# Optimization experiments

Hardware: AMD Instinct MI355X
Metric: run time of the kernel (lower is better)

The kernel has to match this reference:

```python
import jax, jax.numpy as jnp
import numpy as np

BATCH, SEQLEN, D_MODEL, D_STATE = 2, 2048, 512, 64
DT_MIN, DT_MAX = 1e-4, 1e-3


def setup_inputs() -> dict:
    key = jax.random.key(0)
    k1, k2, k3, k4 = jax.random.split(key, 4)
    u = jax.random.normal(k1, (BATCH, SEQLEN, D_MODEL), dtype=jnp.float32)
    # real parts of the complex params B, C (imag parts never affect the output)
    B_re = (jax.random.normal(k2, (D_STATE,), dtype=jnp.float32) / np.float32(np.sqrt(D_STATE)))
    C_re = (jax.random.normal(k3, (D_STATE,), dtype=jnp.float32) / np.float32(np.sqrt(D_STATE)))
    log_dt = jax.random.uniform(k4, (D_MODEL,), minval=np.log(DT_MIN), maxval=np.log(DT_MAX)).astype(jnp.float32)
    D = jnp.ones((D_MODEL,), dtype=jnp.float32)
    return {"u": u, "B_re": B_re, "C_re": C_re, "log_dt": log_dt, "D": D}


def reference(u, B_re, C_re, log_dt, D):
    # u: [B, L, H]; B_re/C_re: [N]; log_dt/D: [H]
    N = B_re.shape[0]
    # buffer: log_A = -0.5 * log(1 + n/N), n = 1..N  (A = exp(log_A) in (0,1])
    log_A = -0.5 * jnp.log1p(jnp.arange(1, N + 1, dtype=jnp.float32) / N)
    A = jnp.exp(log_A)                       # [N]
    delta = jnp.exp(log_dt)                  # [H]
    A_d = jnp.exp(delta[:, None] * A[None, :])          # [H, N]
    B_d = (A_d - 1.0) * B_re[None, :] * delta[:, None]  # [H, N]

    Bsz, L, H = u.shape
    x0 = jnp.zeros((Bsz, H, N), dtype=u.dtype)

    def step(x, u_t):                        # x: [B,H,N], u_t: [B,H]
        x = A_d * x + B_d * u_t[..., None]
        y_t = jnp.einsum('bhn,n->bh', x, C_re) + D * u_t
        return x, y_t

    _, ys = jax.lax.scan(step, x0, jnp.swapaxes(u, 0, 1))  # ys: [L,B,H]
    return jnp.swapaxes(ys, 0, 1)                          # [B,L,H]
```

## Files before the change

kernel.cpp:

```cpp
#include <hip/hip_runtime.h>
#include <math.h>


#define BATCH   2
#define SEQLEN  2048
#define DMODEL  512
#define DSTATE  64
#define T_CHUNK 64
#define NCHUNK  (SEQLEN / T_CHUNK)
#define RT      8

__device__ __forceinline__ float A_cont(int n) {
    return rsqrtf(1.0f + (float)(n + 1) * (1.0f / 64.0f));
}

__global__ __launch_bounds__(256) void k_setup(const float* __restrict__ B_re,
                                               const float* __restrict__ C_re,
                                               const float* __restrict__ log_dt,
                                               const float* __restrict__ D,
                                               float* __restrict__ Kbuf,
                                               float* __restrict__ AdTab,
                                               float* __restrict__ CpowStep) {
    int g = blockIdx.x * blockDim.x + threadIdx.x;
    int h = g & (DMODEL - 1);
    int j = g >> 9;
    float delta = expf(log_dt[h]);
    float dAj = delta * A_cont(j);
    float Adj = expf(dAj);
    AdTab[j * DMODEL + h] = Adj;
    float e8 = Adj * Adj; e8 = e8 * e8; e8 = e8 * e8;
    float p = C_re[j] * Adj;
    #pragma unroll
    for (int i = 0; i < RT; ++i) {
        CpowStep[(i * DSTATE + j) * DMODEL + h] = p;
        p *= e8;
    }
    float acc = (j == 0) ? D[h] : 0.0f;
    for (int n = 0; n < DSTATE; ++n) {
        float dAn = delta * A_cont(n);
        float Bd = expm1f(dAn) * B_re[n] * delta;
        acc = fmaf(C_re[n] * Bd, expf(dAn * (float)j), acc);
    }
    Kbuf[(8 + j) * DMODEL + h] = acc;
    if (j < 8) Kbuf[j * DMODEL + h] = 0.0f;
}

__global__ __launch_bounds__(256) void k_xlocal(const float* __restrict__ u,
                                                const float* __restrict__ B_re,
                                                const float* __restrict__ log_dt,
                                                float* __restrict__ xl) {
    int g = blockIdx.x * blockDim.x + threadIdx.x;
    int lane = g & 63;
    int w = g >> 6;
    int hb = w & 7;
    int ng = (w >> 3) & 7;
    int c  = (w >> 6) & (NCHUNK - 1);
    int b  = w >> 11;
    int h = hb * 64 + lane;
    float delta = expf(log_dt[h]);
    float Ad[8], Bd[8], x[8];
    #pragma unroll
    for (int nn = 0; nn < 8; ++nn) {
        int n = ng * 8 + nn;
        float dA = delta * A_cont(n);
        Ad[nn] = expf(dA);
        Bd[nn] = expm1f(dA) * B_re[n] * delta;
        x[nn] = 0.0f;
    }
    const float* up = u + ((size_t)(b * SEQLEN + c * T_CHUNK)) * DMODEL + h;
    #pragma unroll 4
    for (int s = 0; s < T_CHUNK; ++s) {
        float uv = up[(size_t)s * DMODEL];
        #pragma unroll
        for (int nn = 0; nn < 8; ++nn)
            x[nn] = fmaf(Ad[nn], x[nn], Bd[nn] * uv);
    }
    float* xp = xl + ((size_t)((b * NCHUNK + c) * DSTATE + ng * 8)) * DMODEL + h;
    #pragma unroll
    for (int nn = 0; nn < 8; ++nn) xp[(size_t)nn * DMODEL] = x[nn];
}

__global__ __launch_bounds__(256) void k_scan(const float* __restrict__ log_dt,
                                              float* __restrict__ xl) {
    int g = blockIdx.x * blockDim.x + threadIdx.x;
    int h = g & (DMODEL - 1);
    int n = (g >> 9) & (DSTATE - 1);
    int b = g >> 15;
    float delta = expf(log_dt[h]);
    float ApT = expf(delta * A_cont(n) * (float)T_CHUNK);
    float s = 0.0f;
    float* base = xl + ((size_t)(b * NCHUNK * DSTATE + n)) * DMODEL + h;
    for (int cm1 = 0; cm1 < NCHUNK - 1; ++cm1) {
        float v = base[(size_t)cm1 * DSTATE * DMODEL];
        s = fmaf(ApT, s, v);
        base[(size_t)cm1 * DSTATE * DMODEL] = s;
    }
}

__global__ __launch_bounds__(256) void k_out(const float* __restrict__ u,
                                             const float* __restrict__ Kbuf,
                                             const float* __restrict__ AdTab,
                                             const float* __restrict__ CpowStep,
                                             const float* __restrict__ Sbuf,
                                             float* __restrict__ out) {
    int g = blockIdx.x * blockDim.x + threadIdx.x;
    int h  = g & (DMODEL - 1);
    int it = (g >> 9) & 7;
    int c  = (g >> 12) & (NCHUNK - 1);
    int b  = g >> 17;
    int tp0 = it * RT;

    const float* ubase = u + ((size_t)(b * SEQLEN + c * T_CHUNK)) * DMODEL + h;
    const float* kb = Kbuf + h;

    float acc[RT], kreg[RT];
    #pragma unroll
    for (int i = 0; i < RT; ++i) {
        acc[i] = 0.0f;
        kreg[i] = kb[(size_t)(8 + tp0 + i) * DMODEL];
    }

    for (int s8 = 0; s8 <= it; ++s8) {
        #pragma unroll
        for (int q = 0; q < 8; ++q) {
            int s = s8 * 8 + q;
            float uv = ubase[(size_t)s * DMODEL];
            #pragma unroll
            for (int i = 0; i < RT; ++i) acc[i] = fmaf(kreg[i], uv, acc[i]);
            #pragma unroll
            for (int i = RT - 1; i > 0; --i) kreg[i] = kreg[i - 1];
            kreg[0] = kb[(size_t)(8 + tp0 - s - 1) * DMODEL];
        }
    }

    if (c > 0) {
        const float* sp = Sbuf + ((size_t)((b * NCHUNK + (c - 1)) * DSTATE)) * DMODEL + h;
        const float* ap = AdTab + h;
        const float* cp = CpowStep + (size_t)(it * DSTATE) * DMODEL + h;
        #pragma unroll 4
        for (int n = 0; n < DSTATE; ++n) {
            float Sv  = sp[(size_t)n * DMODEL];
            float Adv = ap[(size_t)n * DMODEL];
            float w   = cp[(size_t)n * DMODEL] * Sv;
            acc[0] += w;
            #pragma unroll
            for (int i = 1; i < RT; ++i) { w *= Adv; acc[i] += w; }
        }
    }

    float* ob = out + ((size_t)(b * SEQLEN + c * T_CHUNK + tp0)) * DMODEL + h;
    #pragma unroll
    for (int i = 0; i < RT; ++i) ob[(size_t)i * DMODEL] = acc[i];
}

extern "C" void kernel_launch(void* const* d_in, const int* in_sizes, int n_in,
                              void* d_out, int out_size, void* d_ws, size_t ws_size,
                              hipStream_t stream) {
    const float* u      = (const float*)d_in[0];
    const float* B_re   = (const float*)d_in[1];
    const float* C_re   = (const float*)d_in[2];
    const float* log_dt = (const float*)d_in[3];
    const float* D      = (const float*)d_in[4];
    float* out = (float*)d_out;
    float* ws  = (float*)d_ws;

    float* Kbuf     = ws;
    float* AdTab    = ws + 36864;
    float* CpowStep = ws + 36864 + 32768;
    float* xl       = ws + 36864 + 32768 + 262144;

    k_setup <<<128, 256, 0, stream>>>(B_re, C_re, log_dt, D, Kbuf, AdTab, CpowStep);
    k_xlocal<<<1024, 256, 0, stream>>>(u, B_re, log_dt, xl);
    k_scan  <<<256, 256, 0, stream>>>(log_dt, xl);
    k_out   <<<1024, 256, 0, stream>>>(u, Kbuf, AdTab, CpowStep, xl, out);
}
```

Baseline: 109.7 us.

## Merge setup and local-scan kernels, batch scan loads, vectorize output with float2

Merges the coefficient-setup and per-chunk local-state kernels into one launch, using block index ranges to pick the role, which removes one launch and its inter-kernel gap. The chunk scan now loads all chunk values into registers before the serial recurrence and stores them afterward, so memory latency is no longer paid inside the dependent loop. The output kernel has each thread handle two adjacent channels with float2 loads and stores, halving the thread count and widening memory accesses, at the cost of more registers per thread and fewer waves.

```diff
diff --git a/kernel.cpp b/kernel.cpp
--- a/kernel.cpp
+++ b/kernel.cpp
@@ -9,92 +9,99 @@
 #define T_CHUNK 64
 #define NCHUNK  (SEQLEN / T_CHUNK)
 #define RT      8
+#define HP      2
 
 __device__ __forceinline__ float A_cont(int n) {
     return rsqrtf(1.0f + (float)(n + 1) * (1.0f / 64.0f));
 }
 
-__global__ __launch_bounds__(256) void k_setup(const float* __restrict__ B_re,
-                                               const float* __restrict__ C_re,
-                                               const float* __restrict__ log_dt,
-                                               const float* __restrict__ D,
-                                               float* __restrict__ Kbuf,
-                                               float* __restrict__ AdTab,
-                                               float* __restrict__ CpowStep) {
-    int g = blockIdx.x * blockDim.x + threadIdx.x;
-    int h = g & (DMODEL - 1);
-    int j = g >> 9;
-    float delta = expf(log_dt[h]);
-    float dAj = delta * A_cont(j);
-    float Adj = expf(dAj);
-    AdTab[j * DMODEL + h] = Adj;
-    float e8 = Adj * Adj; e8 = e8 * e8; e8 = e8 * e8;
-    float p = C_re[j] * Adj;
-    #pragma unroll
-    for (int i = 0; i < RT; ++i) {
-        CpowStep[(i * DSTATE + j) * DMODEL + h] = p;
-        p *= e8;
+__global__ __launch_bounds__(256) void k_prep(const float* __restrict__ u,
+                                              const float* __restrict__ B_re,
+                                              const float* __restrict__ C_re,
+                                              const float* __restrict__ log_dt,
+                                              const float* __restrict__ D,
+                                              float* __restrict__ Kbuf,
+                                              float* __restrict__ AdTab,
+                                              float* __restrict__ CpowStep,
+                                              float* __restrict__ xl) {
+    if (blockIdx.x < 128) {
+        int g = blockIdx.x * 256 + threadIdx.x;
+        int h = g & (DMODEL - 1);
+        int j = g >> 9;
+        float delta = expf(log_dt[h]);
+        float dAj = delta * A_cont(j);
+        float Adj = expf(dAj);
+        AdTab[j * DMODEL + h] = Adj;
+        float e8 = Adj * Adj; e8 = e8 * e8; e8 = e8 * e8;
+        float p = C_re[j] * Adj;
+        #pragma unroll
+        for (int i = 0; i < RT; ++i) {
+            CpowStep[(i * DSTATE + j) * DMODEL + h] = p;
+            p *= e8;
+        }
+        float acc = (j == 0) ? D[h] : 0.0f;
+        for (int n = 0; n < DSTATE; ++n) {
+            float dAn = delta * A_cont(n);
+            float Bd = expm1f(dAn) * B_re[n] * delta;
+            acc = fmaf(C_re[n] * Bd, expf(dAn * (float)j), acc);
+        }
+        Kbuf[(8 + j) * DMODEL + h] = acc;
+        if (j < 8) Kbuf[j * DMODEL + h] = 0.0f;
+    } else {
+        int g = (blockIdx.x - 128) * 256 + threadIdx.x;
+        int lane = g & 63;
+        int w = g >> 6;
+        int hb = w & 7;
+        int ng = (w >> 3) & 7;
+        int c  = (w >> 6) & (NCHUNK - 1);
+        int b  = w >> 11;
+        int h = hb * 64 + lane;
+        float delta = expf(log_dt[h]);
+        float Ad[8], Bd[8], x[8];
+        #pragma unroll
+        for (int nn = 0; nn < 8; ++nn) {
+            int n = ng * 8 + nn;
+            float dA = delta * A_cont(n);
+            Ad[nn] = expf(dA);
+            Bd[nn] = expm1f(dA) * B_re[n] * delta;
+            x[nn] = 0.0f;
+        }
+        const float* up = u + ((size_t)(b * SEQLEN + c * T_CHUNK)) * DMODEL + h;
+        #pragma unroll 4
+        for (int s = 0; s < T_CHUNK; ++s) {
+            float uv = up[(size_t)s * DMODEL];
+            #pragma unroll
+            for (int nn = 0; nn < 8; ++nn)
+                x[nn] = fmaf(Ad[nn], x[nn], Bd[nn] * uv);
+        }
+        float* xp = xl + ((size_t)((b * NCHUNK + c) * DSTATE + ng * 8)) * DMODEL + h;
+        #pragma unroll
+        for (int nn = 0; nn < 8; ++nn) xp[(size_t)nn * DMODEL] = x[nn];
     }
-    float acc = (j == 0) ? D[h] : 0.0f;
-    for (int n = 0; n < DSTATE; ++n) {
-        float dAn = delta * A_cont(n);
-        float Bd = expm1f(dAn) * B_re[n] * delta;
-        acc = fmaf(C_re[n] * Bd, expf(dAn * (float)j), acc);
-    }
-    Kbuf[(8 + j) * DMODEL + h] = acc;
-    if (j < 8) Kbuf[j * DMODEL + h] = 0.0f;
-}
-
-__global__ __launch_bounds__(256) void k_xlocal(const float* __restrict__ u,
-                                                const float* __restrict__ B_re,
-                                                const float* __restrict__ log_dt,
-                                                float* __restrict__ xl) {
-    int g = blockIdx.x * blockDim.x + threadIdx.x;
-    int lane = g & 63;
-    int w = g >> 6;
-    int hb = w & 7;
-    int ng = (w >> 3) & 7;
-    int c  = (w >> 6) & (NCHUNK - 1);
-    int b  = w >> 11;
-    int h = hb * 64 + lane;
-    float delta = expf(log_dt[h]);
-    float Ad[8], Bd[8], x[8];
-    #pragma unroll
-    for (int nn = 0; nn < 8; ++nn) {
-        int n = ng * 8 + nn;
-        float dA = delta * A_cont(n);
-        Ad[nn] = expf(dA);
-        Bd[nn] = expm1f(dA) * B_re[n] * delta;
-        x[nn] = 0.0f;
-    }
-    const float* up = u + ((size_t)(b * SEQLEN + c * T_CHUNK)) * DMODEL + h;
-    #pragma unroll 4
-    for (int s = 0; s < T_CHUNK; ++s) {
-        float uv = up[(size_t)s * DMODEL];
-        #pragma unroll
-        for (int nn = 0; nn < 8; ++nn)
-            x[nn] = fmaf(Ad[nn], x[nn], Bd[nn] * uv);
-    }
-    float* xp = xl + ((size_t)((b * NCHUNK + c) * DSTATE + ng * 8)) * DMODEL + h;
-    #pragma unroll
-    for (int nn = 0; nn < 8; ++nn) xp[(size_t)nn * DMODEL] = x[nn];
 }
 
 __global__ __launch_bounds__(256) void k_scan(const float* __restrict__ log_dt,
                                               float* __restrict__ xl) {
-    int g = blockIdx.x * blockDim.x + threadIdx.x;
+    int g = blockIdx.x * 256 + threadIdx.x;
     int h = g & (DMODEL - 1);
     int n = (g >> 9) & (DSTATE - 1);
     int b = g >> 15;
     float delta = expf(log_dt[h]);
     float ApT = expf(delta * A_cont(n) * (float)T_CHUNK);
+    float* base = xl + ((size_t)(b * NCHUNK * DSTATE + n)) * DMODEL + h;
+    float v[NCHUNK - 1];
+    #pragma unroll
+    for (int c = 0; c < NCHUNK - 1; ++c)
+        v[c] = base[(size_t)c * DSTATE * DMODEL];
     float s = 0.0f;
-    float* base = xl + ((size_t)(b * NCHUNK * DSTATE + n)) * DMODEL + h;
-    for (int cm1 = 0; cm1 < NCHUNK - 1; ++cm1) {
-        float v = base[(size_t)cm1 * DSTATE * DMODEL];
-        s = fmaf(ApT, s, v);
-        base[(size_t)cm1 * DSTATE * DMODEL] = s;
+    #pragma unroll
+    for (int c = 0; c < NCHUNK - 1; ++c) {
+        s = fmaf(ApT, s, v[c]);
+        v[c] = s;
     }
+    #pragma unroll
+    for (int c = 0; c < NCHUNK - 1; ++c)
+        base[(size_t)c * DSTATE * DMODEL] = v[c];
 }
 
 __global__ __launch_bounds__(256) void k_out(const float* __restrict__ u,
@@ -103,54 +110,63 @@
                                              const float* __restrict__ CpowStep,
                                              const float* __restrict__ Sbuf,
                                              float* __restrict__ out) {
-    int g = blockIdx.x * blockDim.x + threadIdx.x;
-    int h  = g & (DMODEL - 1);
-    int it = (g >> 9) & 7;
-    int c  = (g >> 12) & (NCHUNK - 1);
-    int b  = g >> 17;
+    int g = blockIdx.x * 256 + threadIdx.x;
+    int h2 = g & 255;
+    int it = (g >> 8) & 7;
+    int c  = (g >> 11) & (NCHUNK - 1);
+    int b  = g >> 16;
+    int h = h2 * 2;
     int tp0 = it * RT;
+    const int S2 = DMODEL / 2;
 
-    const float* ubase = u + ((size_t)(b * SEQLEN + c * T_CHUNK)) * DMODEL + h;
-    const float* kb = Kbuf + h;
+    const float2* ub = (const float2*)(u + ((size_t)(b * SEQLEN + c * T_CHUNK)) * DMODEL + h);
+    const float2* kb = (const float2*)(Kbuf + h);
 
-    float acc[RT], kreg[RT];
+    float2 acc[RT], kreg[RT];
     #pragma unroll
     for (int i = 0; i < RT; ++i) {
-        acc[i] = 0.0f;
-        kreg[i] = kb[(size_t)(8 + tp0 + i) * DMODEL];
+        acc[i] = make_float2(0.0f, 0.0f);
+        kreg[i] = kb[(size_t)(8 + tp0 + i) * S2];
     }
 
     for (int s8 = 0; s8 <= it; ++s8) {
         #pragma unroll
         for (int q = 0; q < 8; ++q) {
             int s = s8 * 8 + q;
-            float uv = ubase[(size_t)s * DMODEL];
+            float2 uv = ub[(size_t)s * S2];
             #pragma unroll
-            for (int i = 0; i < RT; ++i) acc[i] = fmaf(kreg[i], uv, acc[i]);
+            for (int i = 0; i < RT; ++i) {
+                acc[i].x = fmaf(kreg[i].x, uv.x, acc[i].x);
+                acc[i].y = fmaf(kreg[i].y, uv.y, acc[i].y);
+            }
             #pragma unroll
             for (int i = RT - 1; i > 0; --i) kreg[i] = kreg[i - 1];
-            kreg[0] = kb[(size_t)(8 + tp0 - s - 1) * DMODEL];
+            kreg[0] = kb[(size_t)(8 + tp0 - s - 1) * S2];
         }
     }
 
     if (c > 0) {
-        const float* sp = Sbuf + ((size_t)((b * NCHUNK + (c - 1)) * DSTATE)) * DMODEL + h;
-        const float* ap = AdTab + h;
-        const float* cp = CpowStep + (size_t)(it * DSTATE) * DMODEL + h;
+        const float2* sp = (const float2*)(Sbuf + ((size_t)((b * NCHUNK + (c - 1)) * DSTATE)) * DMODEL + h);
+        const float2* ap = (const float2*)(AdTab + h);
+        const float2* cp = (const float2*)(CpowStep + (size_t)(it * DSTATE) * DMODEL + h);
         #pragma unroll 4
         for (int n = 0; n < DSTATE; ++n) {
-            float Sv  = sp[(size_t)n * DMODEL];
-            float Adv = ap[(size_t)n * DMODEL];
-            float w   = cp[(size_t)n * DMODEL] * Sv;
-            acc[0] += w;
+            float2 Sv  = sp[(size_t)n * S2];
+            float2 Adv = ap[(size_t)n * S2];
+            float2 Cv  = cp[(size_t)n * S2];
+            float2 w = make_float2(Cv.x * Sv.x, Cv.y * Sv.y);
+            acc[0].x += w.x; acc[0].y += w.y;
             #pragma unroll
-            for (int i = 1; i < RT; ++i) { w *= Adv; acc[i] += w; }
+            for (int i = 1; i < RT; ++i) {
+                w.x *= Adv.x; w.y *= Adv.y;
+                acc[i].x += w.x; acc[i].y += w.y;
+            }
         }
     }
 
-    float* ob = out + ((size_t)(b * SEQLEN + c * T_CHUNK + tp0)) * DMODEL + h;
+    float2* ob = (float2*)(out + ((size_t)(b * SEQLEN + c * T_CHUNK + tp0)) * DMODEL + h);
     #pragma unroll
-    for (int i = 0; i < RT; ++i) ob[(size_t)i * DMODEL] = acc[i];
+    for (int i = 0; i < RT; ++i) ob[(size_t)i * S2] = acc[i];
 }
 
 extern "C" void kernel_launch(void* const* d_in, const int* in_sizes, int n_in,
@@ -169,8 +185,7 @@
     float* CpowStep = ws + 36864 + 32768;
     float* xl       = ws + 36864 + 32768 + 262144;
 
-    k_setup <<<128, 256, 0, stream>>>(B_re, C_re, log_dt, D, Kbuf, AdTab, CpowStep);
-    k_xlocal<<<1024, 256, 0, stream>>>(u, B_re, log_dt, xl);
-    k_scan  <<<256, 256, 0, stream>>>(log_dt, xl);
-    k_out   <<<1024, 256, 0, stream>>>(u, Kbuf, AdTab, CpowStep, xl, out);
+    k_prep<<<1152, 256, 0, stream>>>(u, B_re, C_re, log_dt, D, Kbuf, AdTab, CpowStep, xl);
+    k_scan<<<256, 256, 0, stream>>>(log_dt, xl);
+    k_out <<<512, 256, 0, stream>>>(u, Kbuf, AdTab, CpowStep, xl, out);
 }
```

Result: no change. 109.1 us (-0.6%).

## Fuse SSM setup, chunk scan and output into one cooperative kernel

Applied to the files above, without the earlier changes.

Replaces the four separate launches (setup, local chunk states, inter-chunk scan, output) with a single cooperative kernel using grid-wide syncs, cutting launch overhead and inter-kernel gaps. Each thread now handles 16 states or 16 output timesteps instead of 8, halving the grid to 512 blocks. The inter-chunk scan loads all chunk values into registers before the recurrence. The causal convolution is restructured into register-blocked 16x16 tiles. The risks are higher register pressure under launch_bounds(256,2), the cost of the grid syncs, and lower parallelism.

```diff
diff --git a/kernel.cpp b/kernel.cpp
--- a/kernel.cpp
+++ b/kernel.cpp
@@ -1,5 +1,8 @@
 #include <hip/hip_runtime.h>
+#include <hip/hip_cooperative_groups.h>
 #include <math.h>
+
+namespace cg = cooperative_groups;
 
 
 #define BATCH   2
@@ -7,150 +10,156 @@
 #define DMODEL  512
 #define DSTATE  64
 #define T_CHUNK 64
-#define NCHUNK  (SEQLEN / T_CHUNK)
-#define RT      8
+#define NCHUNK  32
+#define RT      16
 
 __device__ __forceinline__ float A_cont(int n) {
     return rsqrtf(1.0f + (float)(n + 1) * (1.0f / 64.0f));
 }
 
-__global__ __launch_bounds__(256) void k_setup(const float* __restrict__ B_re,
-                                               const float* __restrict__ C_re,
-                                               const float* __restrict__ log_dt,
-                                               const float* __restrict__ D,
-                                               float* __restrict__ Kbuf,
-                                               float* __restrict__ AdTab,
-                                               float* __restrict__ CpowStep) {
-    int g = blockIdx.x * blockDim.x + threadIdx.x;
-    int h = g & (DMODEL - 1);
-    int j = g >> 9;
-    float delta = expf(log_dt[h]);
-    float dAj = delta * A_cont(j);
-    float Adj = expf(dAj);
-    AdTab[j * DMODEL + h] = Adj;
-    float e8 = Adj * Adj; e8 = e8 * e8; e8 = e8 * e8;
-    float p = C_re[j] * Adj;
-    #pragma unroll
-    for (int i = 0; i < RT; ++i) {
-        CpowStep[(i * DSTATE + j) * DMODEL + h] = p;
-        p *= e8;
+__global__ __launch_bounds__(256, 2) void k_fused(const float* __restrict__ u,
+                                                  const float* __restrict__ B_re,
+                                                  const float* __restrict__ C_re,
+                                                  const float* __restrict__ log_dt,
+                                                  const float* __restrict__ Dp,
+                                                  float* __restrict__ Kbuf,
+                                                  float* __restrict__ AdTab,
+                                                  float* __restrict__ CpStep,
+                                                  float* __restrict__ xl,
+                                                  float* __restrict__ out) {
+    cg::grid_group grid = cg::this_grid();
+    int tid = blockIdx.x * 256 + threadIdx.x;
+
+    {
+        int h  = tid & (DMODEL - 1);
+        int ng = (tid >> 9) & 3;
+        int c  = (tid >> 11) & (NCHUNK - 1);
+        int b  = tid >> 16;
+        float delta = expf(log_dt[h]);
+        float Ad[16], Bd[16], x[16];
+        #pragma unroll
+        for (int nn = 0; nn < 16; ++nn) {
+            int n = ng * 16 + nn;
+            float dA = delta * A_cont(n);
+            Ad[nn] = expf(dA);
+            Bd[nn] = expm1f(dA) * B_re[n] * delta;
+            x[nn] = 0.0f;
+        }
+        const float* up = u + ((size_t)(b * SEQLEN + c * T_CHUNK)) * DMODEL + h;
+        #pragma unroll 4
+        for (int s = 0; s < T_CHUNK; ++s) {
+            float uv = up[(size_t)s * DMODEL];
+            #pragma unroll
+            for (int nn = 0; nn < 16; ++nn)
+                x[nn] = fmaf(Ad[nn], x[nn], Bd[nn] * uv);
+        }
+        float* xp = xl + ((size_t)((b * NCHUNK + c) * DSTATE + ng * 16)) * DMODEL + h;
+        #pragma unroll
+        for (int nn = 0; nn < 16; ++nn) xp[(size_t)nn * DMODEL] = x[nn];
     }
-    float acc = (j == 0) ? D[h] : 0.0f;
-    for (int n = 0; n < DSTATE; ++n) {
-        float dAn = delta * A_cont(n);
-        float Bd = expm1f(dAn) * B_re[n] * delta;
-        acc = fmaf(C_re[n] * Bd, expf(dAn * (float)j), acc);
-    }
-    Kbuf[(8 + j) * DMODEL + h] = acc;
-    if (j < 8) Kbuf[j * DMODEL + h] = 0.0f;
-}
-
-__global__ __launch_bounds__(256) void k_xlocal(const float* __restrict__ u,
-                                                const float* __restrict__ B_re,
-                                                const float* __restrict__ log_dt,
-                                                float* __restrict__ xl) {
-    int g = blockIdx.x * blockDim.x + threadIdx.x;
-    int lane = g & 63;
-    int w = g >> 6;
-    int hb = w & 7;
-    int ng = (w >> 3) & 7;
-    int c  = (w >> 6) & (NCHUNK - 1);
-    int b  = w >> 11;
-    int h = hb * 64 + lane;
-    float delta = expf(log_dt[h]);
-    float Ad[8], Bd[8], x[8];
-    #pragma unroll
-    for (int nn = 0; nn < 8; ++nn) {
-        int n = ng * 8 + nn;
-        float dA = delta * A_cont(n);
-        Ad[nn] = expf(dA);
-        Bd[nn] = expm1f(dA) * B_re[n] * delta;
-        x[nn] = 0.0f;
-    }
-    const float* up = u + ((size_t)(b * SEQLEN + c * T_CHUNK)) * DMODEL + h;
-    #pragma unroll 4
-    for (int s = 0; s < T_CHUNK; ++s) {
-        float uv = up[(size_t)s * DMODEL];
+    if (tid < 32768) {
+        int h = tid & (DMODEL - 1);
+        int j = tid >> 9;
+        float delta = expf(log_dt[h]);
+        float Adj = expf(delta * A_cont(j));
+        AdTab[j * DMODEL + h] = Adj;
+        float sq = Adj * Adj; sq = sq * sq; sq = sq * sq;
+        float e16 = sq * sq;
+        float p = C_re[j] * Adj;
         #pragma unroll
-        for (int nn = 0; nn < 8; ++nn)
-            x[nn] = fmaf(Ad[nn], x[nn], Bd[nn] * uv);
-    }
-    float* xp = xl + ((size_t)((b * NCHUNK + c) * DSTATE + ng * 8)) * DMODEL + h;
-    #pragma unroll
-    for (int nn = 0; nn < 8; ++nn) xp[(size_t)nn * DMODEL] = x[nn];
-}
-
-__global__ __launch_bounds__(256) void k_scan(const float* __restrict__ log_dt,
-                                              float* __restrict__ xl) {
-    int g = blockIdx.x * blockDim.x + threadIdx.x;
-    int h = g & (DMODEL - 1);
-    int n = (g >> 9) & (DSTATE - 1);
-    int b = g >> 15;
-    float delta = expf(log_dt[h]);
-    float ApT = expf(delta * A_cont(n) * (float)T_CHUNK);
-    float s = 0.0f;
-    float* base = xl + ((size_t)(b * NCHUNK * DSTATE + n)) * DMODEL + h;
-    for (int cm1 = 0; cm1 < NCHUNK - 1; ++cm1) {
-        float v = base[(size_t)cm1 * DSTATE * DMODEL];
-        s = fmaf(ApT, s, v);
-        base[(size_t)cm1 * DSTATE * DMODEL] = s;
-    }
-}
-
-__global__ __launch_bounds__(256) void k_out(const float* __restrict__ u,
-                                             const float* __restrict__ Kbuf,
-                                             const float* __restrict__ AdTab,
-                                             const float* __restrict__ CpowStep,
-                                             const float* __restrict__ Sbuf,
-                                             float* __restrict__ out) {
-    int g = blockIdx.x * blockDim.x + threadIdx.x;
-    int h  = g & (DMODEL - 1);
-    int it = (g >> 9) & 7;
-    int c  = (g >> 12) & (NCHUNK - 1);
-    int b  = g >> 17;
-    int tp0 = it * RT;
-
-    const float* ubase = u + ((size_t)(b * SEQLEN + c * T_CHUNK)) * DMODEL + h;
-    const float* kb = Kbuf + h;
-
-    float acc[RT], kreg[RT];
-    #pragma unroll
-    for (int i = 0; i < RT; ++i) {
-        acc[i] = 0.0f;
-        kreg[i] = kb[(size_t)(8 + tp0 + i) * DMODEL];
+        for (int i = 0; i < 4; ++i) {
+            CpStep[(i * DSTATE + j) * DMODEL + h] = p;
+            p *= e16;
+        }
+        float acc = (j == 0) ? Dp[h] : 0.0f;
+        for (int n = 0; n < DSTATE; ++n) {
+            float dAn = delta * A_cont(n);
+            float Bd = expm1f(dAn) * B_re[n] * delta;
+            acc = fmaf(C_re[n] * Bd, expf(dAn * (float)j), acc);
+        }
+        Kbuf[j * DMODEL + h] = acc;
     }
 
-    for (int s8 = 0; s8 <= it; ++s8) {
+    grid.sync();
+
+    if (tid < 65536) {
+        int h = tid & (DMODEL - 1);
+        int n = (tid >> 9) & (DSTATE - 1);
+        int b = tid >> 15;
+        float delta = expf(log_dt[h]);
+        float ApT = expf(delta * A_cont(n) * (float)T_CHUNK);
+        float* base = xl + ((size_t)(b * NCHUNK * DSTATE + n)) * DMODEL + h;
+        float v[NCHUNK - 1];
         #pragma unroll
-        for (int q = 0; q < 8; ++q) {
-            int s = s8 * 8 + q;
-            float uv = ubase[(size_t)s * DMODEL];
-            #pragma unroll
-            for (int i = 0; i < RT; ++i) acc[i] = fmaf(kreg[i], uv, acc[i]);
-            #pragma unroll
-            for (int i = RT - 1; i > 0; --i) kreg[i] = kreg[i - 1];
-            kreg[0] = kb[(size_t)(8 + tp0 - s - 1) * DMODEL];
-        }
+        for (int c = 0; c < NCHUNK - 1; ++c)
+            v[c] = base[(size_t)c * DSTATE * DMODEL];
+        float s = 0.0f;
+        #pragma unroll
+        for (int c = 0; c < NCHUNK - 1; ++c) { s = fmaf(ApT, s, v[c]); v[c] = s; }
+        #pragma unroll
+        for (int c = 0; c < NCHUNK - 1; ++c)
+            base[(size_t)c * DSTATE * DMODEL] = v[c];
     }
 
-    if (c > 0) {
-        const float* sp = Sbuf + ((size_t)((b * NCHUNK + (c - 1)) * DSTATE)) * DMODEL + h;
-        const float* ap = AdTab + h;
-        const float* cp = CpowStep + (size_t)(it * DSTATE) * DMODEL + h;
-        #pragma unroll 4
-        for (int n = 0; n < DSTATE; ++n) {
-            float Sv  = sp[(size_t)n * DMODEL];
-            float Adv = ap[(size_t)n * DMODEL];
-            float w   = cp[(size_t)n * DMODEL] * Sv;
-            acc[0] += w;
+    grid.sync();
+
+    {
+        int h   = tid & (DMODEL - 1);
+        int it4 = (tid >> 9) & 3;
+        int c   = (tid >> 11) & (NCHUNK - 1);
+        int b   = tid >> 16;
+        int tp0 = it4 * RT;
+
+        const float* ub = u + ((size_t)(b * SEQLEN + c * T_CHUNK)) * DMODEL + h;
+        const float* kb = Kbuf + h;
+
+        float acc[RT];
+        #pragma unroll
+        for (int i = 0; i < RT; ++i) acc[i] = 0.0f;
+
+        for (int sb = 0; sb < it4; ++sb) {
+            float ureg[16], krow[31];
+            int base = tp0 - sb * 16 - 15;
             #pragma unroll
-            for (int i = 1; i < RT; ++i) { w *= Adv; acc[i] += w; }
+            for (int q = 0; q < 16; ++q) ureg[q] = ub[(size_t)(sb * 16 + q) * DMODEL];
+            #pragma unroll
+            for (int j = 0; j < 31; ++j) krow[j] = kb[(size_t)(base + j) * DMODEL];
+            #pragma unroll
+            for (int q = 0; q < 16; ++q)
+                #pragma unroll
+                for (int i = 0; i < RT; ++i)
+                    acc[i] = fmaf(krow[i - q + 15], ureg[q], acc[i]);
         }
+        {
+            float ureg[16], krow[16];
+            #pragma unroll
+            for (int q = 0; q < 16; ++q) ureg[q] = ub[(size_t)(tp0 + q) * DMODEL];
+            #pragma unroll
+            for (int j = 0; j < 16; ++j) krow[j] = kb[(size_t)j * DMODEL];
+            #pragma unroll
+            for (int q = 0; q < 16; ++q)
+                #pragma unroll
+                for (int i = 0; i < RT; ++i)
+                    if (i >= q) acc[i] = fmaf(krow[i - q], ureg[q], acc[i]);
+        }
+        if (c > 0) {
+            const float* sp = xl + ((size_t)((b * NCHUNK + (c - 1)) * DSTATE)) * DMODEL + h;
+            const float* ap = AdTab + h;
+            const float* cp = CpStep + (size_t)(it4 * DSTATE) * DMODEL + h;
+            #pragma unroll 4
+            for (int n = 0; n < DSTATE; ++n) {
+                float Sv  = sp[(size_t)n * DMODEL];
+                float Adv = ap[(size_t)n * DMODEL];
+                float w   = cp[(size_t)n * DMODEL] * Sv;
+                acc[0] += w;
+                #pragma unroll
+                for (int i = 1; i < RT; ++i) { w *= Adv; acc[i] += w; }
+            }
+        }
+        float* ob = out + ((size_t)(b * SEQLEN + c * T_CHUNK + tp0)) * DMODEL + h;
+        #pragma unroll
+        for (int i = 0; i < RT; ++i) ob[(size_t)i * DMODEL] = acc[i];
     }
-
-    float* ob = out + ((size_t)(b * SEQLEN + c * T_CHUNK + tp0)) * DMODEL + h;
-    #pragma unroll
-    for (int i = 0; i < RT; ++i) ob[(size_t)i * DMODEL] = acc[i];
 }
 
 extern "C" void kernel_launch(void* const* d_in, const int* in_sizes, int n_in,
@@ -164,13 +173,12 @@
     float* out = (float*)d_out;
     float* ws  = (float*)d_ws;
 
-    float* Kbuf     = ws;
-    float* AdTab    = ws + 36864;
-    float* CpowStep = ws + 36864 + 32768;
-    float* xl       = ws + 36864 + 32768 + 262144;
+    float* Kbuf   = ws;
+    float* AdTab  = ws + 32768;
+    float* CpStep = ws + 65536;
+    float* xl     = ws + 65536 + 131072;
 
-    k_setup <<<128, 256, 0, stream>>>(B_re, C_re, log_dt, D, Kbuf, AdTab, CpowStep);
-    k_xlocal<<<1024, 256, 0, stream>>>(u, B_re, log_dt, xl);
-    k_scan  <<<256, 256, 0, stream>>>(log_dt, xl);
-    k_out   <<<1024, 256, 0, stream>>>(u, Kbuf, AdTab, CpowStep, xl, out);
+    void* args[] = {(void*)&u, (void*)&B_re, (void*)&C_re, (void*)&log_dt, (void*)&D,
+                    (void*)&Kbuf, (void*)&AdTab, (void*)&CpStep, (void*)&xl, (void*)&out};
+    hipLaunchCooperativeKernel((const void*)k_fused, dim3(512), dim3(256), args, 0, stream);
 }
```

Result: slower. 233.6 us (+112.8%).
